# Performance work log

Hardware: AMD Instinct MI355X
Metric: run time of the kernel (lower is better)

Reference implementation:

```python
import jax, jax.numpy as jnp
import numpy as np

B, S, D_IN, D_H, D_OUT = 32, 1024, 512, 512, 512
N_HEADS, K_NEI = 2, 3
LN_EPS = 1e-5


def _layernorm(x, g, b):
    mu = x.mean(-1, keepdims=True)
    xc = x - mu
    var = (xc * xc).mean(-1, keepdims=True)
    return xc * jax.lax.rsqrt(var + LN_EPS) * g + b


def setup_inputs() -> dict:
    key = jax.random.key(0)
    ks = jax.random.split(key, 8)
    sc = 0.02
    rn = lambda k, shape: jax.random.normal(k, shape, jnp.float32) * sc
    return {
        "x": jax.random.normal(ks[0], (B, S, D_IN), jnp.float32),
        "enc_w": rn(ks[1], (D_H, D_IN)), "enc_b": jnp.zeros((D_H,), jnp.float32),
        "in_w": rn(ks[2], (3 * D_H, D_H)), "in_b": jnp.zeros((3 * D_H,), jnp.float32),
        "out_w": rn(ks[3], (D_H, D_H)), "out_b": jnp.zeros((D_H,), jnp.float32),
        "ln1_g": jnp.ones((D_H,), jnp.float32), "ln1_b": jnp.zeros((D_H,), jnp.float32),
        "ffn_w1": rn(ks[4], (2 * D_H, D_H)), "ffn_b1": jnp.zeros((2 * D_H,), jnp.float32),
        "ffn_w2": rn(ks[5], (D_H, 2 * D_H)), "ffn_b2": jnp.zeros((D_H,), jnp.float32),
        "gc_w": rn(ks[6], (D_H, 2 * D_H)), "gc_b": jnp.zeros((D_H,), jnp.float32),
        "ln2_g": jnp.ones((D_H,), jnp.float32), "ln2_b": jnp.zeros((D_H,), jnp.float32),
        "dec_w": rn(ks[7], (D_OUT, D_H)), "dec_b": jnp.zeros((D_OUT,), jnp.float32),
    }


def reference(x, enc_w, enc_b, in_w, in_b, out_w, out_b, ln1_g, ln1_b,
              ffn_w1, ffn_b1, ffn_w2, ffn_b2, gc_w, gc_b, ln2_g, ln2_b,
              dec_w, dec_b):
    # --- encoder ---
    h = jax.nn.relu(x @ enc_w.T + enc_b)                          # [B,S,Dh]

    # --- ElevateH0toH1: self-attention + LN + residual FFN ---
    qkv = h @ in_w.T + in_b                                       # [B,S,3Dh]
    q, k, v = jnp.split(qkv, 3, axis=-1)
    dh = D_H // N_HEADS
    heads = lambda t: t.reshape(B, S, N_HEADS, dh).transpose(0, 2, 1, 3)
    q, k, v = heads(q), heads(k), heads(v)
    scores = jnp.einsum("bhqd,bhkd->bhqk", q, k) / jnp.sqrt(jnp.float32(dh))
    attn = jax.nn.softmax(scores, axis=-1)
    ctx = jnp.einsum("bhqk,bhkd->bhqd", attn, v)
    ctx = ctx.transpose(0, 2, 1, 3).reshape(B, S, D_H)
    attn_out = ctx @ out_w.T + out_b
    x1 = _layernorm(h + attn_out, ln1_g, ln1_b)
    x1 = x1 + (jax.nn.relu(x1 @ ffn_w1.T + ffn_b1) @ ffn_w2.T + ffn_b2)

    # --- ElevateH1toH2: symmetric KNN adjacency from cosine similarity ---
    nrm = x1 / jnp.maximum(jnp.linalg.norm(x1, axis=-1, keepdims=True), 1e-12)
    sim = jnp.einsum("bid,bjd->bij", nrm, nrm)                    # [B,S,S]
    kk = min(K_NEI, S - 1)
    _, idx = jax.lax.top_k(sim, kk + 1)                           # [B,S,k+1] (incl. self)
    mask = jnp.zeros((B, S, S), bool).at[
        jnp.arange(B)[:, None, None], jnp.arange(S)[None, :, None], idx
    ].set(True)
    mask = mask & ~jnp.eye(S, dtype=bool)                         # drop self edges
    mask = mask | mask.transpose(0, 2, 1)                         # symmetrize
    adj = jnp.where(mask, sim, jnp.float32(0.0))

    nsum = jnp.einsum("bij,bjd->bid", adj, x1)
    cnt = jnp.maximum(adj.sum(-1, keepdims=True), jnp.float32(1.0))
    combined = jnp.concatenate([x1, nsum / cnt], axis=-1)         # [B,S,2Dh]
    out = combined @ gc_w.T + gc_b
    x2 = _layernorm(x1 + out, ln2_g, ln2_b)

    # --- pool + decoder ---
    return x2.mean(axis=1) @ dec_w.T + dec_b                      # [B,D_OUT]
```

## Files before the change

### kernel.cpp

```cpp
#include <hip/hip_runtime.h>
#include <hip/hip_bf16.h>
#include <math.h>

typedef unsigned short u16;
typedef __attribute__((ext_vector_type(8))) short bfrag;
typedef __attribute__((ext_vector_type(4))) float facc;
typedef const __attribute__((address_space(1))) void* gaddr_t;
typedef __attribute__((address_space(3))) void* laddr_t;

#define F_RELU   1
#define F_ROWSC  4
#define F_SIMSC  8
#define F_RESID2 32

__device__ __forceinline__ u16 f2bf(float f) {
  __hip_bfloat16 h = __float2bfloat16(f);
  return *reinterpret_cast<u16*>(&h);
}
__device__ __forceinline__ float bf2f(u16 u) {
  __hip_bfloat16 h = *reinterpret_cast<__hip_bfloat16*>(&u);
  return __bfloat162float(h);
}
__device__ __forceinline__ float wsum(float v) {
#pragma unroll
  for (int o = 32; o; o >>= 1) v += __shfl_xor(v, o);
  return v;
}
__device__ __forceinline__ float wmaxf(float v) {
#pragma unroll
  for (int o = 32; o; o >>= 1) v = fmaxf(v, __shfl_xor(v, o));
  return v;
}

struct GSeg {
  const u16* A; const u16* B;
  long sA, sB;
  int lda, ldb, K;
  int hA, hB;
};

__global__ __launch_bounds__(256)
void bgemm_k(GSeg s0, GSeg s1, GSeg s2,
             const float* __restrict__ bias,
             const u16* __restrict__ residH, const u16* __restrict__ residL,
             const float* __restrict__ rsc, const float* __restrict__ csc,
             float* __restrict__ Cf, u16* __restrict__ Cb, u16* __restrict__ Cb2,
             int ldc, long sC, int hC, int headBits, int sS,
             float alpha, int flags, int Mstore)
{
  const int zAll = blockIdx.z;
  const int hIdx = headBits ? (zAll & 1) : 0;
  const int z    = headBits ? (zAll >> 1) : zAll;
  const long cofs = (long)z * sC + (long)hIdx * hC;
  const float* rs = rsc ? rsc + (long)z * sS : nullptr;
  const float* cs = csc ? csc + (long)z * sS : nullptr;

  __shared__ u16 As[2][128 * 64];
  __shared__ u16 Bs[2][128 * 64];

  const int tid  = threadIdx.x;
  const int wave = tid >> 6, lane = tid & 63;
  const int m0 = blockIdx.x * 128, n0 = blockIdx.y * 128;
  const int wrow = (wave >> 1) * 64, wcol = (wave & 1) * 64;

  const u16* ApS[3]; const u16* BpS[3]; int ldaS[3], ldbS[3];
  ApS[0] = s0.A + (long)z * s0.sA + (long)hIdx * s0.hA;
  BpS[0] = s0.B + (long)z * s0.sB + (long)hIdx * s0.hB;
  ldaS[0] = s0.lda; ldbS[0] = s0.ldb;
  ApS[1] = s1.A ? s1.A + (long)z * s1.sA + (long)hIdx * s1.hA : nullptr;
  BpS[1] = s1.B ? s1.B + (long)z * s1.sB + (long)hIdx * s1.hB : nullptr;
  ldaS[1] = s1.lda; ldbS[1] = s1.ldb;
  ApS[2] = s2.A ? s2.A + (long)z * s2.sA + (long)hIdx * s2.hA : nullptr;
  BpS[2] = s2.B ? s2.B + (long)z * s2.sB + (long)hIdx * s2.hB : nullptr;
  ldaS[2] = s2.lda; ldbS[2] = s2.ldb;
  const int n0i = s0.K >> 6, n1i = n0i + (s1.K >> 6);
  const int nIt = n1i + (s2.K >> 6);

  const int lrow = lane >> 3;
  const int lgrp = lane & 7;

  facc acc[4][4];
#pragma unroll
  for (int i = 0; i < 4; ++i)
#pragma unroll
    for (int j = 0; j < 4; ++j) acc[i][j] = (facc)(0.f);

  const int r16 = lane & 15, gq = lane >> 4;

  auto stage = [&](int buf, int it) {
    int sidx, base;
    if (it < n0i)      { sidx = 0; base = 0; }
    else if (it < n1i) { sidx = 1; base = n0i; }
    else               { sidx = 2; base = n1i; }
    const int k0 = (it - base) << 6;
    const u16* Ab = ApS[sidx];
    const u16* Bb = BpS[sidx];
    const int la = ldaS[sidx], lb = ldbS[sidx];
#pragma unroll
    for (int ss = 0; ss < 4; ++ss) {
      int rloc = wave * 32 + ss * 8;
      int row  = rloc + lrow;
      int g    = lgrp ^ ((row >> 1) & 7);
      __builtin_amdgcn_global_load_lds(
          (gaddr_t)(const void*)(Ab + (long)(m0 + row) * la + k0 + g * 8),
          (laddr_t)(As[buf] + rloc * 64), 16, 0, 0);
      __builtin_amdgcn_global_load_lds(
          (gaddr_t)(const void*)(Bb + (long)(n0 + row) * lb + k0 + g * 8),
          (laddr_t)(Bs[buf] + rloc * 64), 16, 0, 0);
    }
  };

  stage(0, 0);
  for (int it = 0; it < nIt; ++it) {
    const int buf = it & 1;
    __syncthreads();
    if (it + 1 < nIt) stage(buf ^ 1, it + 1);

#pragma unroll
    for (int kk = 0; kk < 2; ++kk) {
      bfrag af[4], bb[4];
#pragma unroll
      for (int mt = 0; mt < 4; ++mt) {
        int r = wrow + mt * 16 + r16;
        int slot = (kk * 4 + gq) ^ ((r >> 1) & 7);
        af[mt] = *(const bfrag*)&As[buf][r * 64 + slot * 8];
      }
#pragma unroll
      for (int nt = 0; nt < 4; ++nt) {
        int r = wcol + nt * 16 + r16;
        int slot = (kk * 4 + gq) ^ ((r >> 1) & 7);
        bb[nt] = *(const bfrag*)&Bs[buf][r * 64 + slot * 8];
      }
#pragma unroll
      for (int mt = 0; mt < 4; ++mt)
#pragma unroll
        for (int nt = 0; nt < 4; ++nt)
          acc[mt][nt] = __builtin_amdgcn_mfma_f32_16x16x32_bf16(
              af[mt], bb[nt], acc[mt][nt], 0, 0, 0);
    }
  }

#pragma unroll
  for (int mt = 0; mt < 4; ++mt) {
#pragma unroll
    for (int nt = 0; nt < 4; ++nt) {
#pragma unroll
      for (int r = 0; r < 4; ++r) {
        int gm = m0 + wrow + mt * 16 + gq * 4 + r;
        int gn = n0 + wcol + nt * 16 + r16;
        if (gm >= Mstore) continue;
        float v = acc[mt][nt][r] * alpha;
        long ci = cofs + (long)gm * ldc + gn;
        if (flags & F_SIMSC)  v *= rs[gm] * cs[gn];
        if (flags & F_ROWSC)  v *= rs[gm];
        if (bias)             v += bias[gn];
        if (flags & F_RESID2) v += bf2f(residH[ci]) + bf2f(residL[ci]);
        if (flags & F_RELU)   v = fmaxf(v, 0.f);
        if (Cf) Cf[ci] = v;
        if (Cb) {
          u16 hv = f2bf(v);
          Cb[ci] = hv;
          if (Cb2) Cb2[ci] = f2bf(v - bf2f(hv));
        }
      }
    }
  }
}

__global__ __launch_bounds__(256)
void castbf_k(const float* __restrict__ in, u16* __restrict__ out, int n)
{
  int i = blockIdx.x * 256 + threadIdx.x;
  if (i < n) out[i] = f2bf(in[i]);
}

__global__ __launch_bounds__(256)
void castw_k(const float* w0, const float* w1, const float* w2,
             const float* w3, const float* w4, const float* w5,
             const float* w6, u16* __restrict__ dst)
{
  int i = blockIdx.x * 256 + threadIdx.x;
  const float* s; int off;
  if      (i < 262144)  { s = w0; off = 0; }
  else if (i < 1048576) { s = w1; off = 262144; }
  else if (i < 1310720) { s = w2; off = 1048576; }
  else if (i < 1835008) { s = w3; off = 1310720; }
  else if (i < 2359296) { s = w4; off = 1835008; }
  else if (i < 2883584) { s = w5; off = 2359296; }
  else                  { s = w6; off = 2883584; }
  dst[i] = f2bf(s[i - off]);
}

__global__ __launch_bounds__(256)
void ln1_k(const u16* __restrict__ a, const u16* __restrict__ b,
           const float* __restrict__ g, const float* __restrict__ be,
           u16* __restrict__ oh, u16* __restrict__ ol)
{
  long base = (long)blockIdx.x * 512;
  int t = threadIdx.x;
  float v0 = bf2f(a[base + t])       + bf2f(b[base + t]);
  float v1 = bf2f(a[base + t + 256]) + bf2f(b[base + t + 256]);
  __shared__ float red[4], red2[4];
  float s = wsum(v0 + v1);
  if ((t & 63) == 0) red[t >> 6] = s;
  __syncthreads();
  float mean = (red[0] + red[1] + red[2] + red[3]) * (1.f / 512.f);
  float c0 = v0 - mean, c1 = v1 - mean;
  float ss = wsum(c0 * c0 + c1 * c1);
  if ((t & 63) == 0) red2[t >> 6] = ss;
  __syncthreads();
  float var = (red2[0] + red2[1] + red2[2] + red2[3]) * (1.f / 512.f);
  float rstd = rsqrtf(var + 1e-5f);
  float o0 = c0 * rstd * g[t]       + be[t];
  float o1 = c1 * rstd * g[t + 256] + be[t + 256];
  u16 h0 = f2bf(o0), h1 = f2bf(o1);
  oh[base + t] = h0;       oh[base + t + 256] = h1;
  ol[base + t] = f2bf(o0 - bf2f(h0));
  ol[base + t + 256] = f2bf(o1 - bf2f(h1));
}

__global__ __launch_bounds__(256)
void ln2_k(const u16* __restrict__ hi, const u16* __restrict__ lo,
           const u16* __restrict__ b, const float* __restrict__ g,
           const float* __restrict__ be, u16* __restrict__ ob)
{
  long base = (long)blockIdx.x * 512;
  int t = threadIdx.x;
  float v0 = bf2f(hi[base + t])       + bf2f(lo[base + t])       + bf2f(b[base + t]);
  float v1 = bf2f(hi[base + t + 256]) + bf2f(lo[base + t + 256]) + bf2f(b[base + t + 256]);
  __shared__ float red[4], red2[4];
  float s = wsum(v0 + v1);
  if ((t & 63) == 0) red[t >> 6] = s;
  __syncthreads();
  float mean = (red[0] + red[1] + red[2] + red[3]) * (1.f / 512.f);
  float c0 = v0 - mean, c1 = v1 - mean;
  float ss = wsum(c0 * c0 + c1 * c1);
  if ((t & 63) == 0) red2[t >> 6] = ss;
  __syncthreads();
  float var = (red2[0] + red2[1] + red2[2] + red2[3]) * (1.f / 512.f);
  float rstd = rsqrtf(var + 1e-5f);
  ob[base + t]       = f2bf(c0 * rstd * g[t]       + be[t]);
  ob[base + t + 256] = f2bf(c1 * rstd * g[t + 256] + be[t + 256]);
}

__global__ __launch_bounds__(256)
void rownorm_k(const u16* __restrict__ hi, const u16* __restrict__ lo,
               float* __restrict__ invn)
{
  long base = (long)blockIdx.x * 512;
  int t = threadIdx.x;
  float v0 = bf2f(hi[base + t])       + bf2f(lo[base + t]);
  float v1 = bf2f(hi[base + t + 256]) + bf2f(lo[base + t + 256]);
  __shared__ float red[4];
  float s = wsum(v0 * v0 + v1 * v1);
  if ((t & 63) == 0) red[t >> 6] = s;
  __syncthreads();
  if (t == 0) {
    float tot = red[0] + red[1] + red[2] + red[3];
    invn[blockIdx.x] = 1.f / fmaxf(sqrtf(tot), 1e-12f);
  }
}

__global__ __launch_bounds__(256)
void softmaxu_k(u16* __restrict__ sc)
{
  long row = blockIdx.x;
  u16* p = sc + row * 1024;
  int t = threadIdx.x;
  float v[4];
#pragma unroll
  for (int i = 0; i < 4; ++i) v[i] = bf2f(p[t + 256 * i]);
  __shared__ float redm[4], redsum[4];
  float m4 = fmaxf(fmaxf(v[0], v[1]), fmaxf(v[2], v[3]));
  float wm = wmaxf(m4);
  if ((t & 63) == 0) redm[t >> 6] = wm;
  __syncthreads();
  float MX = fmaxf(fmaxf(redm[0], redm[1]), fmaxf(redm[2], redm[3]));
  float s = 0.f;
#pragma unroll
  for (int i = 0; i < 4; ++i) { v[i] = __expf(v[i] - MX); s += v[i]; }
  float ws_ = wsum(s);
  if ((t & 63) == 0) redsum[t >> 6] = ws_;
  __syncthreads();
  float inv = 1.f / (redsum[0] + redsum[1] + redsum[2] + redsum[3]);
#pragma unroll
  for (int i = 0; i < 4; ++i) p[t + 256 * i] = f2bf(v[i] * inv);
}

__global__ __launch_bounds__(256)
void transp_k(const u16* __restrict__ in, u16* __restrict__ out,
              int inStride, int outStride, long sIn, long sOut,
              int hIn, int headBits)
{
  const int zAll = blockIdx.z;
  const int h  = headBits ? (zAll & 1) : 0;
  const int zb = headBits ? (zAll >> 1) : zAll;
  const u16* src = in + (long)zb * sIn + (long)h * hIn;
  u16* dst = out + (long)zAll * sOut;
  const int r0 = blockIdx.x * 64, c0 = blockIdx.y * 64;
  __shared__ u16 tile[64][66];
  const int t = threadIdx.x;
#pragma unroll
  for (int p = 0; p < 16; ++p) {
    int idx = p * 256 + t;
    int r = idx >> 6, c = idx & 63;
    tile[r][c] = src[(long)(r0 + r) * inStride + c0 + c];
  }
  __syncthreads();
#pragma unroll
  for (int p = 0; p < 16; ++p) {
    int idx = p * 256 + t;
    int c = idx >> 6, r = idx & 63;
    dst[(long)(c0 + c) * outStride + r0 + r] = tile[r][c];
  }
}

__global__ __launch_bounds__(256)
void topk_k(const u16* __restrict__ sim, int* __restrict__ idx4)
{
  __shared__ float row[1024];
  __shared__ float bv[4];
  __shared__ int   bidx[4];
  long r = blockIdx.x;
  const u16* p = sim + r * 1024;
  int t = threadIdx.x;
  for (int i = t; i < 1024; i += 256) row[i] = bf2f(p[i]);
  __syncthreads();
  int c0 = -1, c1 = -1, c2 = -1, c3 = -1;
#pragma unroll
  for (int pass = 0; pass < 4; ++pass) {
    float best = -INFINITY;
    int bi = 1 << 30;
#pragma unroll
    for (int q = 0; q < 4; ++q) {
      int j = t + q * 256;
      if (j == c0 || j == c1 || j == c2 || j == c3) continue;
      float v = row[j];
      if (v > best || (v == best && j < bi)) { best = v; bi = j; }
    }
#pragma unroll
    for (int off = 32; off; off >>= 1) {
      float ov = __shfl_down(best, off);
      int   oi = __shfl_down(bi, off);
      if (ov > best || (ov == best && oi < bi)) { best = ov; bi = oi; }
    }
    if ((t & 63) == 0) { bv[t >> 6] = best; bidx[t >> 6] = bi; }
    __syncthreads();
    if (t == 0) {
      float bb = bv[0]; int ii = bidx[0];
#pragma unroll
      for (int w = 1; w < 4; ++w)
        if (bv[w] > bb || (bv[w] == bb && bidx[w] < ii)) { bb = bv[w]; ii = bidx[w]; }
      bidx[0] = ii;
    }
    __syncthreads();
    int sel = bidx[0];
    if (pass == 0) c0 = sel; else if (pass == 1) c1 = sel;
    else if (pass == 2) c2 = sel; else c3 = sel;
    __syncthreads();
  }
  if (t == 0) { int* q = idx4 + r * 4; q[0] = c0; q[1] = c1; q[2] = c2; q[3] = c3; }
}

__global__ __launch_bounds__(256)
void adjbf_k(u16* __restrict__ simadj, const int* __restrict__ idx4,
             float* __restrict__ invcnt)
{
  long row = blockIdx.x;
  int b = (int)(row >> 10);
  int i = (int)(row & 1023);
  u16* prow = simadj + row * 1024;
  const int* my = idx4 + row * 4;
  int m0 = my[0], m1 = my[1], m2 = my[2], m3 = my[3];
  int t = threadIdx.x;
  float lsum = 0.f;
  for (int j = t; j < 1024; j += 256) {
    float v = bf2f(prow[j]);
    bool present = false;
    if (j != i) {
      present = (j == m0) | (j == m1) | (j == m2) | (j == m3);
      if (!present) {
        const int* oj = idx4 + (((long)b << 10) + j) * 4;
        present = (oj[0] == i) | (oj[1] == i) | (oj[2] == i) | (oj[3] == i);
      }
    }
    float a = present ? v : 0.f;
    prow[j] = present ? prow[j] : (u16)0;
    lsum += a;
  }
  __shared__ float red[4];
  float s = wsum(lsum);
  if ((t & 63) == 0) red[t >> 6] = s;
  __syncthreads();
  if (t == 0) {
    float tot = red[0] + red[1] + red[2] + red[3];
    invcnt[row] = 1.f / fmaxf(tot, 1.f);
  }
}

__global__ __launch_bounds__(256)
void poolbf_k(const u16* __restrict__ x2, u16* __restrict__ pooled)
{
  int i = blockIdx.x * 256 + threadIdx.x;
  int b = i >> 9, d = i & 511;
  float s = 0.f;
  if (b < 32) {
    const u16* p = x2 + ((long)b << 10) * 512 + d;
    for (int sdx = 0; sdx < 1024; ++sdx) s += bf2f(p[(long)sdx * 512]);
    s *= (1.f / 1024.f);
  }
  pooled[i] = f2bf(s);
}

static inline GSeg mkseg(const u16* A, const u16* B, int K, int lda, int ldb,
                         long sA = 0, long sB = 0, int hA = 0, int hB = 0)
{
  GSeg s; s.A = A; s.B = B; s.K = K; s.lda = lda; s.ldb = ldb;
  s.sA = sA; s.sB = sB; s.hA = hA; s.hB = hB; return s;
}

static inline void bgemm(hipStream_t st, GSeg s0, GSeg s1, GSeg s2,
    const float* bias, const u16* residH, const u16* residL,
    const float* rsc, const float* csc, float* Cf, u16* Cb, u16* Cb2,
    int M, int N, int ldc, long sC, int hC, int headBits, int sS,
    float alpha, int flags, int nz, int Mstore = -1)
{
  dim3 g(M / 128, N / 128, nz);
  bgemm_k<<<g, 256, 0, st>>>(s0, s1, s2, bias, residH, residL,
                             rsc, csc, Cf, Cb, Cb2, ldc, sC, hC, headBits,
                             sS, alpha, flags, Mstore < 0 ? M : Mstore);
}

extern "C" void kernel_launch(void* const* d_in, const int* in_sizes, int n_in,
                              void* d_out, int out_size, void* d_ws, size_t ws_size,
                              hipStream_t stream)
{
  (void)in_sizes; (void)n_in; (void)out_size;
  const float* x     = (const float*)d_in[0];
  const float* enc_w = (const float*)d_in[1];
  const float* enc_b = (const float*)d_in[2];
  const float* in_w  = (const float*)d_in[3];
  const float* in_b  = (const float*)d_in[4];
  const float* out_w = (const float*)d_in[5];
  const float* out_b = (const float*)d_in[6];
  const float* ln1_g = (const float*)d_in[7];
  const float* ln1_b = (const float*)d_in[8];
  const float* fw1   = (const float*)d_in[9];
  const float* fb1   = (const float*)d_in[10];
  const float* fw2   = (const float*)d_in[11];
  const float* fb2   = (const float*)d_in[12];
  const float* gc_w  = (const float*)d_in[13];
  const float* gc_b  = (const float*)d_in[14];
  const float* ln2_g = (const float*)d_in[15];
  const float* ln2_b = (const float*)d_in[16];
  const float* dec_w = (const float*)d_in[17];
  const float* dec_b = (const float*)d_in[18];
  float* out = (float*)d_out;

  char* base = (char*)d_ws;
  u16*  bf1  = (u16*)(base);
  u16*  lob  = (u16*)(base + 33554432);
  u16*  bf2  = (u16*)(base + 67108864);
  u16*  wgt  = (u16*)(base + 100663296);
  float* invn    = (float*)(base + 106954752);
  float* invcnt  = (float*)(base + 107085824);
  u16*   pooledb = (u16*)(base + 107216896);
  int*   idx4    = (int*)(base + 107347968);
  char*  scr     = base + 107872256;
  const size_t need = 107872256 + 83886080;
  if (ws_size < need) return;

  u16* encw = wgt;
  u16* inw  = wgt + 262144;
  u16* outw = wgt + 1048576;
  u16* fw1b = wgt + 1310720;
  u16* fw2b = wgt + 1835008;
  u16* gcwb = wgt + 2359296;
  u16* decw = wgt + 2883584;

  const int Mtok = 32768;
  GSeg Z = mkseg(nullptr, nullptr, 0, 0, 0);

  u16* xbf = (u16*)scr;
  castbf_k<<<65536, 256, 0, stream>>>(x, xbf, 16777216);
  castw_k<<<12288, 256, 0, stream>>>(enc_w, in_w, out_w, fw1, fw2, gc_w, dec_w, wgt);

  bgemm(stream, mkseg(xbf, encw, 512, 512, 512), Z, Z,
        enc_b, nullptr, nullptr, nullptr, nullptr, nullptr, bf1, nullptr,
        Mtok, 512, 512, 0, 0, 0, 0, 1.f, F_RELU, 1);

  for (int c = 0; c < 4; ++c) {
    long row0 = (long)c * 8192;
    u16* qkvc = (u16*)scr;
    u16* sco  = (u16*)(scr + 25165824);
    u16* vT   = (u16*)(scr + 58720256);
    bgemm(stream, mkseg(bf1 + row0 * 512, inw, 512, 512, 512), Z, Z,
          in_b, nullptr, nullptr, nullptr, nullptr, nullptr, qkvc, nullptr,
          8192, 1536, 1536, 0, 0, 0, 0, 1.f, 0, 1);
    bgemm(stream, mkseg(qkvc, qkvc + 512, 256, 1536, 1536,
                        1572864, 1572864, 256, 256), Z, Z,
          nullptr, nullptr, nullptr, nullptr, nullptr, nullptr, sco, nullptr,
          1024, 1024, 1024, 2097152, 1048576, 1, 0, 0.0625f, 0, 16);
    softmaxu_k<<<16384, 256, 0, stream>>>(sco);
    transp_k<<<dim3(16, 4, 16), 256, 0, stream>>>(
        qkvc + 1024, vT, 1536, 1024, 1572864, 262144, 256, 1);
    bgemm(stream, mkseg(sco, vT, 1024, 1024, 1024,
                        2097152, 524288, 1048576, 262144), Z, Z,
          nullptr, nullptr, nullptr, nullptr, nullptr, nullptr,
          bf2 + row0 * 512, nullptr,
          1024, 256, 512, 524288, 256, 1, 0, 1.f, 0, 16);
  }

  u16* aoc = (u16*)scr;
  bgemm(stream, mkseg(bf2, outw, 512, 512, 512), Z, Z,
        out_b, nullptr, nullptr, nullptr, nullptr, nullptr, aoc, nullptr,
        Mtok, 512, 512, 0, 0, 0, 0, 1.f, 0, 1);

  ln1_k<<<Mtok, 256, 0, stream>>>(bf1, aoc, ln1_g, ln1_b, bf1, lob);

  u16* mid = (u16*)scr;
  bgemm(stream, mkseg(bf1, fw1b, 512, 512, 512), Z, Z,
        fb1, nullptr, nullptr, nullptr, nullptr, nullptr, mid, nullptr,
        Mtok, 1024, 1024, 0, 0, 0, 0, 1.f, F_RELU, 1);
  bgemm(stream, mkseg(mid, fw2b, 1024, 1024, 1024), Z, Z,
        fb2, bf1, lob, nullptr, nullptr, nullptr, bf1, lob,
        Mtok, 512, 512, 0, 0, 0, 0, 1.f, F_RESID2, 1);

  rownorm_k<<<Mtok, 256, 0, stream>>>(bf1, lob, invn);

  u16* simadj = (u16*)scr;
  u16* x1T    = (u16*)(scr + 33554432);
  transp_k<<<dim3(16, 8, 32), 256, 0, stream>>>(bf1, x1T, 512, 1024,
                                                524288, 524288, 0, 0);
  for (int g = 0; g < 2; ++g) {
    long row0 = (long)g * 16384;
    bgemm(stream,
          mkseg(bf1 + row0 * 512, bf1 + row0 * 512, 512, 512, 512, 524288, 524288),
          Z, Z, nullptr, nullptr, nullptr, invn + row0, invn + row0,
          nullptr, simadj, nullptr,
          1024, 1024, 1024, 1048576, 0, 0, 1024, 1.f, F_SIMSC, 16);
    topk_k<<<16384, 256, 0, stream>>>(simadj, idx4 + row0 * 4);
    adjbf_k<<<16384, 256, 0, stream>>>(simadj, idx4 + row0 * 4, invcnt + row0);
    bgemm(stream, mkseg(simadj, x1T + row0 * 512, 1024, 1024, 1024,
                        1048576, 524288), Z, Z,
          nullptr, nullptr, nullptr, invcnt + row0, nullptr, nullptr,
          bf2 + row0 * 512, nullptr,
          1024, 512, 512, 524288, 0, 0, 1024, 1.f, F_ROWSC, 16);
  }

  u16* gch = (u16*)scr;
  bgemm(stream, mkseg(bf1, gcwb, 512, 512, 1024),
        mkseg(bf2, gcwb + 512, 512, 512, 1024), Z,
        gc_b, nullptr, nullptr, nullptr, nullptr, nullptr, gch, nullptr,
        Mtok, 512, 512, 0, 0, 0, 0, 1.f, 0, 1);

  ln2_k<<<Mtok, 256, 0, stream>>>(bf1, lob, gch, ln2_g, ln2_b, bf2);

  poolbf_k<<<256, 256, 0, stream>>>(bf2, pooledb);
  bgemm(stream, mkseg(pooledb, decw, 512, 512, 512), Z, Z,
        dec_b, nullptr, nullptr, nullptr, nullptr, out, nullptr, nullptr,
        128, 512, 512, 0, 0, 0, 0, 1.f, 0, 1, 32);
}
```

Measured before the change: 1.534 ms.

## Switch GEMM to 32x32x16 MFMA and compute V transposed via GEMM

The GEMM inner loop now uses 32x32x16 bf16 MFMA instructions with 2x2 accumulator tiles per wave instead of 4x4 tiles of 16x16x32, which halves the number of LDS fragment loads per MFMA and issues fewer, larger instructions. The V projection is split out of the per-chunk QKV GEMM and computed once for all tokens as W_v·h^T, giving V already transposed, with a new per-row bias flag. This removes the separate transpose kernel in the attention loop. The cost is a different epilogue layout, a large extra scratch buffer reused as V^T, and a changed stride in the PV GEMM.

Measured after the change: 1.497 ms. 1.02x faster.

```diff
diff --git a/kernel.cpp b/kernel.cpp
--- a/kernel.cpp
+++ b/kernel.cpp
@@ -4,7 +4,7 @@
 
 typedef unsigned short u16;
 typedef __attribute__((ext_vector_type(8))) short bfrag;
-typedef __attribute__((ext_vector_type(4))) float facc;
+typedef __attribute__((ext_vector_type(16))) float facc16;
 typedef const __attribute__((address_space(1))) void* gaddr_t;
 typedef __attribute__((address_space(3))) void* laddr_t;
 
@@ -12,6 +12,7 @@
 #define F_ROWSC  4
 #define F_SIMSC  8
 #define F_RESID2 32
+#define F_BIASM  64
 
 __device__ __forceinline__ u16 f2bf(float f) {
   __hip_bfloat16 h = __float2bfloat16(f);
@@ -79,13 +80,13 @@
   const int lrow = lane >> 3;
   const int lgrp = lane & 7;
 
-  facc acc[4][4];
-#pragma unroll
-  for (int i = 0; i < 4; ++i)
-#pragma unroll
-    for (int j = 0; j < 4; ++j) acc[i][j] = (facc)(0.f);
-
-  const int r16 = lane & 15, gq = lane >> 4;
+  facc16 acc[2][2];
+#pragma unroll
+  for (int i = 0; i < 2; ++i)
+#pragma unroll
+    for (int j = 0; j < 2; ++j) acc[i][j] = (facc16)(0.f);
+
+  const int l31 = lane & 31, l5 = lane >> 5;
 
   auto stage = [&](int buf, int it) {
     int sidx, base;
@@ -117,43 +118,44 @@
     if (it + 1 < nIt) stage(buf ^ 1, it + 1);
 
 #pragma unroll
-    for (int kk = 0; kk < 2; ++kk) {
-      bfrag af[4], bb[4];
-#pragma unroll
-      for (int mt = 0; mt < 4; ++mt) {
-        int r = wrow + mt * 16 + r16;
-        int slot = (kk * 4 + gq) ^ ((r >> 1) & 7);
+    for (int ks = 0; ks < 4; ++ks) {
+      const int gg = ks * 2 + l5;
+      bfrag af[2], bb[2];
+#pragma unroll
+      for (int mt = 0; mt < 2; ++mt) {
+        int r = wrow + mt * 32 + l31;
+        int slot = gg ^ ((r >> 1) & 7);
         af[mt] = *(const bfrag*)&As[buf][r * 64 + slot * 8];
       }
 #pragma unroll
-      for (int nt = 0; nt < 4; ++nt) {
-        int r = wcol + nt * 16 + r16;
-        int slot = (kk * 4 + gq) ^ ((r >> 1) & 7);
+      for (int nt = 0; nt < 2; ++nt) {
+        int r = wcol + nt * 32 + l31;
+        int slot = gg ^ ((r >> 1) & 7);
         bb[nt] = *(const bfrag*)&Bs[buf][r * 64 + slot * 8];
       }
 #pragma unroll
-      for (int mt = 0; mt < 4; ++mt)
-#pragma unroll
-        for (int nt = 0; nt < 4; ++nt)
-          acc[mt][nt] = __builtin_amdgcn_mfma_f32_16x16x32_bf16(
+      for (int mt = 0; mt < 2; ++mt)
+#pragma unroll
+        for (int nt = 0; nt < 2; ++nt)
+          acc[mt][nt] = __builtin_amdgcn_mfma_f32_32x32x16_bf16(
               af[mt], bb[nt], acc[mt][nt], 0, 0, 0);
     }
   }
 
 #pragma unroll
-  for (int mt = 0; mt < 4; ++mt) {
-#pragma unroll
-    for (int nt = 0; nt < 4; ++nt) {
-#pragma unroll
-      for (int r = 0; r < 4; ++r) {
-        int gm = m0 + wrow + mt * 16 + gq * 4 + r;
-        int gn = n0 + wcol + nt * 16 + r16;
+  for (int mt = 0; mt < 2; ++mt) {
+#pragma unroll
+    for (int nt = 0; nt < 2; ++nt) {
+#pragma unroll
+      for (int rg = 0; rg < 16; ++rg) {
+        int gm = m0 + wrow + mt * 32 + (rg & 3) + 8 * (rg >> 2) + 4 * l5;
+        int gn = n0 + wcol + nt * 32 + l31;
         if (gm >= Mstore) continue;
-        float v = acc[mt][nt][r] * alpha;
+        float v = acc[mt][nt][rg] * alpha;
         long ci = cofs + (long)gm * ldc + gn;
         if (flags & F_SIMSC)  v *= rs[gm] * cs[gn];
         if (flags & F_ROWSC)  v *= rs[gm];
-        if (bias)             v += bias[gn];
+        if (bias)             v += bias[(flags & F_BIASM) ? gm : gn];
         if (flags & F_RESID2) v += bf2f(residH[ci]) + bf2f(residL[ci]);
         if (flags & F_RELU)   v = fmaxf(v, 0.f);
         if (Cf) Cf[ci] = v;
@@ -289,14 +291,11 @@
 
 __global__ __launch_bounds__(256)
 void transp_k(const u16* __restrict__ in, u16* __restrict__ out,
-              int inStride, int outStride, long sIn, long sOut,
-              int hIn, int headBits)
-{
-  const int zAll = blockIdx.z;
-  const int h  = headBits ? (zAll & 1) : 0;
-  const int zb = headBits ? (zAll >> 1) : zAll;
-  const u16* src = in + (long)zb * sIn + (long)h * hIn;
-  u16* dst = out + (long)zAll * sOut;
+              int inStride, int outStride, long sIn, long sOut)
+{
+  const int z = blockIdx.z;
+  const u16* src = in + (long)z * sIn;
+  u16* dst = out + (long)z * sOut;
   const int r0 = blockIdx.x * 64, c0 = blockIdx.y * 64;
   __shared__ u16 tile[64][66];
   const int t = threadIdx.x;
@@ -489,23 +488,24 @@
         enc_b, nullptr, nullptr, nullptr, nullptr, nullptr, bf1, nullptr,
         Mtok, 512, 512, 0, 0, 0, 0, 1.f, F_RELU, 1);
 
+  bgemm(stream, mkseg(inw + 524288, bf1, 512, 512, 512), Z, Z,
+        in_b + 1024, nullptr, nullptr, nullptr, nullptr, nullptr,
+        lob, nullptr, 512, Mtok, Mtok, 0, 0, 0, 0, 1.f, F_BIASM, 1);
+
   for (int c = 0; c < 4; ++c) {
     long row0 = (long)c * 8192;
-    u16* qkvc = (u16*)scr;
-    u16* sco  = (u16*)(scr + 25165824);
-    u16* vT   = (u16*)(scr + 58720256);
+    u16* qkc = (u16*)scr;
+    u16* sco = (u16*)(scr + 16777216);
     bgemm(stream, mkseg(bf1 + row0 * 512, inw, 512, 512, 512), Z, Z,
-          in_b, nullptr, nullptr, nullptr, nullptr, nullptr, qkvc, nullptr,
-          8192, 1536, 1536, 0, 0, 0, 0, 1.f, 0, 1);
-    bgemm(stream, mkseg(qkvc, qkvc + 512, 256, 1536, 1536,
-                        1572864, 1572864, 256, 256), Z, Z,
+          in_b, nullptr, nullptr, nullptr, nullptr, nullptr, qkc, nullptr,
+          8192, 1024, 1024, 0, 0, 0, 0, 1.f, 0, 1);
+    bgemm(stream, mkseg(qkc, qkc + 512, 256, 1024, 1024,
+                        1048576, 1048576, 256, 256), Z, Z,
           nullptr, nullptr, nullptr, nullptr, nullptr, nullptr, sco, nullptr,
           1024, 1024, 1024, 2097152, 1048576, 1, 0, 0.0625f, 0, 16);
     softmaxu_k<<<16384, 256, 0, stream>>>(sco);
-    transp_k<<<dim3(16, 4, 16), 256, 0, stream>>>(
-        qkvc + 1024, vT, 1536, 1024, 1572864, 262144, 256, 1);
-    bgemm(stream, mkseg(sco, vT, 1024, 1024, 1024,
-                        2097152, 524288, 1048576, 262144), Z, Z,
+    bgemm(stream, mkseg(sco, lob + (row0 >> 10) * 1024, 1024, 1024, Mtok,
+                        2097152, 1024, 1048576, 8388608), Z, Z,
           nullptr, nullptr, nullptr, nullptr, nullptr, nullptr,
           bf2 + row0 * 512, nullptr,
           1024, 256, 512, 524288, 256, 1, 0, 1.f, 0, 16);
@@ -531,7 +531,7 @@
   u16* simadj = (u16*)scr;
   u16* x1T    = (u16*)(scr + 33554432);
   transp_k<<<dim3(16, 8, 32), 256, 0, stream>>>(bf1, x1T, 512, 1024,
-                                                524288, 524288, 0, 0);
+                                                524288, 524288);
   for (int g = 0; g < 2; ++g) {
     long row0 = (long)g * 16384;
     bgemm(stream,
```
